# Kernel optimization log

Hardware: AMD Instinct MI355X
Metric: run time of the kernel (lower is better)

## Reference

```python
import jax, jax.numpy as jnp
import numpy as np

NUM_NODES = 94
SEQ_LEN = 784
OUT_CLASSES = 10
ALPHA = 0.5
GAMMA = 0.1
OMEGA = 2.0 * np.pi / 28.0
H = 1.0
INV_SQRT_N = 1.0 / np.sqrt(NUM_NODES)


def _xavier(key, shape):
    fan_in, fan_out = shape[1], shape[0]
    limit = np.sqrt(6.0 / (fan_in + fan_out))
    return jax.random.uniform(key, shape, jnp.float32, -limit, limit)


def setup_inputs() -> dict:
    key = jax.random.key(0)
    k_in, k_ih, k_hh, k_ro = jax.random.split(key, 4)
    batch = 1024
    return {
        "input_sequence": jax.random.normal(k_in, (batch, SEQ_LEN), jnp.float32),
        "w_ih": _xavier(k_ih, (NUM_NODES, 1)),   # Linear(1 -> N) weight
        "b_ih": jnp.zeros((NUM_NODES,), jnp.float32),
        "w_hh": _xavier(k_hh, (NUM_NODES, NUM_NODES)),  # Linear(N -> N) weight
        "b_hh": jnp.zeros((NUM_NODES,), jnp.float32),
        "w_ro": _xavier(k_ro, (OUT_CLASSES, NUM_NODES)),  # readout weight
        "b_ro": jnp.zeros((OUT_CLASSES,), jnp.float32),
    }


def reference(input_sequence, w_ih, b_ih, w_hh, b_hh, w_ro, b_ro):
    batch = input_sequence.shape[0]
    # precompute external drive for all steps: [T, B, N]
    # W_ih(s_t) with input_dim=1 is an outer product: s_t * w_ih[:,0] + b_ih
    s = input_sequence.T  # [T, B]
    w_ih_vec = w_ih[:, 0]  # [N]

    def step(carry, s_t):
        x, y = carry
        I_ext = s_t[:, None] * w_ih_vec[None, :] + b_ih  # [B, N]
        I_rec = y @ w_hh.T + b_hh                        # [B, N]
        A = (I_ext + I_rec) * INV_SQRT_N
        accel = ALPHA * jnp.tanh(A) - 2.0 * GAMMA * y - (OMEGA ** 2) * x
        x_new = x + H * y
        y_new = y + H * accel
        return (x_new, y_new), None

    x0 = jnp.zeros((batch, NUM_NODES), jnp.float32)
    y0 = jnp.zeros((batch, NUM_NODES), jnp.float32)
    (x_final, _), _ = jax.lax.scan(step, (x0, y0), s)
    return x_final @ w_ro.T + b_ro  # [B, 10]
```

## Files before the change

### kernel.cpp

```cpp
#include <hip/hip_runtime.h>
#include <math.h>

#define NUM_NODES 94
#define SEQ_LEN 784
#define OUT_CLASSES 10
#define EPB 16
#define NW 4
#define SP 788
#define YP 104

#define TWO_GAMMA 0.2f
#define OM2 0.0503551324598949f
#define INV_SQRT_N 0.103142124625879
#define LOG2E 1.4426950408889634
#define WSCALE ((float)(2.0 * INV_SQRT_N * LOG2E))

typedef _Float16 half8 __attribute__((ext_vector_type(8)));
typedef _Float16 half4 __attribute__((ext_vector_type(4)));
typedef _Float16 half2v __attribute__((ext_vector_type(2)));
typedef float    floatx4 __attribute__((ext_vector_type(4)));
typedef float    f2 __attribute__((ext_vector_type(2)));

__global__
__attribute__((amdgpu_flat_work_group_size(NW*64, NW*64)))
void horn_kernel(
    const float* __restrict__ input,
    const float* __restrict__ w_ih,
    const float* __restrict__ b_ih,
    const float* __restrict__ w_hh,
    const float* __restrict__ b_hh,
    const float* __restrict__ w_ro,
    const float* __restrict__ b_ro,
    float* __restrict__ out)
{
    __shared__ __align__(16) float    sinl[EPB * SP];
    __shared__ __align__(16) _Float16 ybuf[2][EPB * YP];

    const int tid  = threadIdx.x;
    const int w    = tid >> 6;
    const int lane = tid & 63;
    const int e    = lane & 15;
    const int h    = lane >> 4;
    const int bb   = blockIdx.x;

    const int  S      = 4 + (w >> 1);
    const int  sthalf = w & 1;
    const bool shpub  = ((h >> 1) == sthalf);
    const bool duty   = (w == 0 && h == 3);
    const bool tail53 = (w == 3 && h == 3);

    {
        const floatx4* in4 = (const floatx4*)(input + (size_t)bb * EPB * SEQ_LEN);
        for (int idx = tid; idx < EPB * (SEQ_LEN / 4); idx += NW * 64) {
            int ee = idx / (SEQ_LEN / 4);
            int cc = idx - ee * (SEQ_LEN / 4);
            *(floatx4*)&sinl[ee * SP + 4 * cc] = in4[idx];
        }
    }
    for (int i = tid; i < (2 * EPB * YP) / 2; i += NW * 64) ((float*)ybuf)[i] = 0.0f;
    __syncthreads();
    if (tid < EPB) {
        const float s0 = sinl[tid * SP];
        half2v v; v[0] = (_Float16)s0; v[1] = (_Float16)1.0f;
        *(half2v*)&ybuf[0][tid * YP + NUM_NODES] = v;
    }
    __syncthreads();

    #define LOAD_A(ROW, A0, A1, A2) do {                                           \
        const int arow = (ROW);                                                    \
        _Pragma("unroll")                                                          \
        for (int i = 0; i < 8; ++i) {                                              \
            const int k = 8 * h + i;                                               \
            float v0 = 0.0f, v1 = 0.0f, v2 = 0.0f;                                 \
            if (arow < NUM_NODES) {                                                \
                v0 = w_hh[arow * NUM_NODES + k] * WSCALE;                          \
                v1 = w_hh[arow * NUM_NODES + k + 32] * WSCALE;                     \
                const int k2 = k + 64;                                             \
                if      (k2 <  NUM_NODES) v2 = w_hh[arow * NUM_NODES + k2] * WSCALE; \
                else if (k2 == NUM_NODES) v2 = w_ih[arow] * WSCALE;                \
                else                      v2 = (b_ih[arow] + b_hh[arow]) * WSCALE; \
            }                                                                      \
            (A0)[i] = (_Float16)v0; (A1)[i] = (_Float16)v1; (A2)[i] = (_Float16)v2;\
        }                                                                          \
    } while (0)

    half8 AO0, AO1, AO2, AS0, AS1, AS2;
    LOAD_A(16 * w + e, AO0, AO1, AO2);
    LOAD_A(16 * S + e, AS0, AS1, AS2);
    #undef LOAD_A

    f2 xo01 = {0,0}, xo23 = {0,0}, yo01 = {0,0}, yo23 = {0,0};
    f2 xs01 = {0,0}, xs23 = {0,0}, ys01 = {0,0}, ys23 = {0,0};

    const f2 no2 = {-OM2, -OM2};
    const f2 p82 = {1.0f - TWO_GAMMA, 1.0f - TWO_GAMMA};
    const f2 h05 = {0.5f, 0.5f};
    const floatx4 zf4 = {0,0,0,0};

    #define HSTEP(RP, WP, T_) do {                                                 \
        const _Float16* yb = &ybuf[RP][e * YP + 8 * h];                            \
        half8 B0 = *(const half8*)(yb);                                            \
        half8 B1 = *(const half8*)(yb + 32);                                       \
        half8 B2 = *(const half8*)(yb + 64);                                       \
        float sn = 0.0f;                                                           \
        if (duty) {                                                                \
            const int tn = ((T_) + 1 < SEQ_LEN) ? (T_) + 1 : (SEQ_LEN - 1);        \
            sn = sinl[e * SP + tn];                                                \
        }                                                                          \
                         \
        f2 qo0 = no2 * xo01 + h05;  qo0 = p82 * yo01 + qo0;                        \
        f2 qo1 = no2 * xo23 + h05;  qo1 = p82 * yo23 + qo1;                        \
        f2 qs0 = no2 * xs01 + h05;  qs0 = p82 * ys01 + qs0;                        \
        f2 qs1 = no2 * xs23 + h05;  qs1 = p82 * ys23 + qs1;                        \
        xo01 += yo01;  xo23 += yo23;  xs01 += ys01;  xs23 += ys23;                 \
                                    \
        floatx4 dO  = __builtin_amdgcn_mfma_f32_16x16x32_f16(AO0, B0, zf4, 0, 0, 0); \
        floatx4 dOp = __builtin_amdgcn_mfma_f32_16x16x32_f16(AO1, B1, zf4, 0, 0, 0); \
        floatx4 dS  = __builtin_amdgcn_mfma_f32_16x16x32_f16(AS0, B0, zf4, 0, 0, 0); \
        floatx4 dSp = __builtin_amdgcn_mfma_f32_16x16x32_f16(AS1, B1, zf4, 0, 0, 0); \
        dO = __builtin_amdgcn_mfma_f32_16x16x32_f16(AO2, B2, dO, 0, 0, 0);         \
        dS = __builtin_amdgcn_mfma_f32_16x16x32_f16(AS2, B2, dS, 0, 0, 0);         \
        dO += dOp;  dS += dSp;                          \
        f2 r0, r1;                                                                 \
        r0[0] = __builtin_amdgcn_rcpf(__builtin_amdgcn_exp2f(dO[0]) + 1.0f);       \
        r0[1] = __builtin_amdgcn_rcpf(__builtin_amdgcn_exp2f(dO[1]) + 1.0f);       \
        r1[0] = __builtin_amdgcn_rcpf(__builtin_amdgcn_exp2f(dO[2]) + 1.0f);       \
        r1[1] = __builtin_amdgcn_rcpf(__builtin_amdgcn_exp2f(dO[3]) + 1.0f);       \
        yo01 = qo0 - r0;  yo23 = qo1 - r1;                                         \
        half4 yh;                                                                  \
        yh[0] = (_Float16)yo01[0]; yh[1] = (_Float16)yo01[1];                      \
        yh[2] = (_Float16)yo23[0]; yh[3] = (_Float16)yo23[1];                      \
        *(half4*)&ybuf[WP][e * YP + 16 * w + 4 * h] = yh;       \
        f2 s0_, s1_;                                                               \
        s0_[0] = __builtin_amdgcn_rcpf(__builtin_amdgcn_exp2f(dS[0]) + 1.0f);      \
        s0_[1] = __builtin_amdgcn_rcpf(__builtin_amdgcn_exp2f(dS[1]) + 1.0f);      \
        s1_[0] = __builtin_amdgcn_rcpf(__builtin_amdgcn_exp2f(dS[2]) + 1.0f);      \
        s1_[1] = __builtin_amdgcn_rcpf(__builtin_amdgcn_exp2f(dS[3]) + 1.0f);      \
        ys01 = qs0 - s0_;  ys23 = qs1 - s1_;                                       \
        half4 yhs;                                                                 \
        yhs[0] = (_Float16)ys01[0]; yhs[1] = (_Float16)ys01[1];                    \
        yhs[2] = (_Float16)ys23[0]; yhs[3] = (_Float16)ys23[1];                    \
        if (shpub) {                                                               \
            if (tail53) {                                                          \
                half2v yt; yt[0] = yhs[0]; yt[1] = yhs[1];         \
                *(half2v*)&ybuf[WP][e * YP + 92] = yt;                             \
            } else {                                                               \
                *(half4*)&ybuf[WP][e * YP + 16 * S + 4 * h] = yhs;                 \
            }                                                                      \
        }                                                                          \
        if (duty) {                                                                \
            half2v sv; sv[0] = (_Float16)sn; sv[1] = (_Float16)1.0f;               \
            *(half2v*)&ybuf[WP][e * YP + NUM_NODES] = sv;                          \
        }                                                                          \
        __syncthreads();                                                           \
    } while (0)

    for (int t = 0; t < SEQ_LEN; t += 2) {
        HSTEP(0, 1, t);
        HSTEP(1, 0, t + 1);
    }
    #undef HSTEP

    float* xsh = sinl;
    {
        floatx4 xv;
        xv[0] = xo01[0]; xv[1] = xo01[1]; xv[2] = xo23[0]; xv[3] = xo23[1];
        *(floatx4*)&xsh[e * 100 + 16 * w + 4 * h] = xv;
        if (shpub) {
            floatx4 xw;
            xw[0] = xs01[0]; xw[1] = xs01[1]; xw[2] = xs23[0]; xw[3] = xs23[1];
            *(floatx4*)&xsh[e * 100 + 16 * S + 4 * h] = xw;
        }
    }
    __syncthreads();

    if (tid < EPB * OUT_CLASSES) {
        const int ee = tid / OUT_CLASSES;
        const int c  = tid - ee * OUT_CLASSES;
        float acc = b_ro[c];
        #pragma unroll 2
        for (int r = 0; r < NUM_NODES; ++r)
            acc += xsh[ee * 100 + r] * w_ro[c * NUM_NODES + r];
        out[((size_t)bb * EPB + ee) * OUT_CLASSES + c] = acc;
    }
}

extern "C" void kernel_launch(void* const* d_in, const int* in_sizes, int n_in,
                              void* d_out, int out_size, void* d_ws, size_t ws_size,
                              hipStream_t stream) {
    const float* input = (const float*)d_in[0];
    const float* w_ih  = (const float*)d_in[1];
    const float* b_ih  = (const float*)d_in[2];
    const float* w_hh  = (const float*)d_in[3];
    const float* b_hh  = (const float*)d_in[4];
    const float* w_ro  = (const float*)d_in[5];
    const float* b_ro  = (const float*)d_in[6];
    float* out = (float*)d_out;

    const int batch = in_sizes[0] / SEQ_LEN;
    dim3 grid(batch / EPB);
    dim3 block(NW * 64);

    hipLaunchKernelGGL(horn_kernel, grid, block, 0, stream,
                       input, w_ih, b_ih, w_hh, b_hh, w_ro, b_ro, out);
}
```

Before: 344.6 us.

## Ping-pong two 16-element teams per block to overlap MFMA and tanh phases

Doubles the block to 512 threads with two teams of 16 batch elements each, and alternates the phases. One team runs its MFMA recurrence matmul while the other runs its transcendental/state-update phase, separated by barriers. The goal is to hide the serial latency within each step by interleaving independent work. Input staging now covers half the sequence at a time to fit shared memory, with a global-memory fallback at the boundary. Shared-memory padding is added against bank conflicts, and work for the extra rows is split across waves. The grid is halved, which reduces parallelism across CUs, and the block now pays two barriers per timestep.

```diff
diff --git a/kernel.cpp b/kernel.cpp
--- a/kernel.cpp
+++ b/kernel.cpp
@@ -4,10 +4,11 @@
 #define NUM_NODES 94
 #define SEQ_LEN 784
 #define OUT_CLASSES 10
-#define EPB 16
-#define NW 4
-#define SP 788
+#define EPB 32
+#define SP 396
+#define THALF 392
 #define YP 104
+#define TEAMSZ 1664
 
 #define TWO_GAMMA 0.2f
 #define OM2 0.0503551324598949f
@@ -22,7 +23,7 @@
 typedef float    f2 __attribute__((ext_vector_type(2)));
 
 __global__
-__attribute__((amdgpu_flat_work_group_size(NW*64, NW*64)))
+__attribute__((amdgpu_flat_work_group_size(512, 512)))
 void horn_kernel(
     const float* __restrict__ input,
     const float* __restrict__ w_ih,
@@ -34,7 +35,7 @@
     float* __restrict__ out)
 {
     __shared__ __align__(16) float    sinl[EPB * SP];
-    __shared__ __align__(16) _Float16 ybuf[2][EPB * YP];
+    __shared__ __align__(16) _Float16 ybuf[2 * TEAMSZ];
 
     const int tid  = threadIdx.x;
     const int w    = tid >> 6;
@@ -43,28 +44,34 @@
     const int h    = lane >> 4;
     const int bb   = blockIdx.x;
 
-    const int  S      = 4 + (w >> 1);
-    const int  sthalf = w & 1;
-    const bool shpub  = ((h >> 1) == sthalf);
-    const bool duty   = (w == 0 && h == 3);
-    const bool tail53 = (w == 3 && h == 3);
+    const int  team = w >> 2;
+    const int  ww   = w & 3;
+    const int  S    = 4 + (ww >> 1);
+    const int  p    = ww & 1;
+    const bool duty = (ww == 3 && h == 3);
+
+    const int Eloc = 16 * team + e;
+    _Float16* ybT  = ybuf + team * TEAMSZ;
+    const int eoff = 104 * e + 4 * (e >> 3);
 
     {
-        const floatx4* in4 = (const floatx4*)(input + (size_t)bb * EPB * SEQ_LEN);
-        for (int idx = tid; idx < EPB * (SEQ_LEN / 4); idx += NW * 64) {
-            int ee = idx / (SEQ_LEN / 4);
-            int cc = idx - ee * (SEQ_LEN / 4);
-            *(floatx4*)&sinl[ee * SP + 4 * cc] = in4[idx];
-        }
-    }
-    for (int i = tid; i < (2 * EPB * YP) / 2; i += NW * 64) ((float*)ybuf)[i] = 0.0f;
+        const float* src = input + (size_t)bb * EPB * SEQ_LEN;
+        for (int idx = tid; idx < EPB * (THALF / 4); idx += 512) {
+            int ee = idx / (THALF / 4);
+            int cc = idx - ee * (THALF / 4);
+            *(floatx4*)&sinl[ee * SP + 4 * cc] =
+                *(const floatx4*)(src + (size_t)ee * SEQ_LEN + 4 * cc);
+        }
+    }
+    for (int i = tid; i < (2 * TEAMSZ) / 2; i += 512) ((float*)ybuf)[i] = 0.0f;
     __syncthreads();
     if (tid < EPB) {
+        const int tm = tid >> 4, ee = tid & 15;
+        const int eo = 104 * ee + 4 * (ee >> 3);
         const float s0 = sinl[tid * SP];
         half2v v; v[0] = (_Float16)s0; v[1] = (_Float16)1.0f;
-        *(half2v*)&ybuf[0][tid * YP + NUM_NODES] = v;
-    }
-    __syncthreads();
+        *(half2v*)&ybuf[tm * TEAMSZ + eo + NUM_NODES] = v;
+    }
 
     #define LOAD_A(ROW, A0, A1, A2) do {                                           \
         const int arow = (ROW);                                                    \
@@ -85,91 +92,108 @@
     } while (0)
 
     half8 AO0, AO1, AO2, AS0, AS1, AS2;
-    LOAD_A(16 * w + e, AO0, AO1, AO2);
-    LOAD_A(16 * S + e, AS0, AS1, AS2);
+    LOAD_A(16 * ww + e, AO0, AO1, AO2);
+    LOAD_A(16 * S + e,  AS0, AS1, AS2);
     #undef LOAD_A
 
-    f2 xo01 = {0,0}, xo23 = {0,0}, yo01 = {0,0}, yo23 = {0,0};
-    f2 xs01 = {0,0}, xs23 = {0,0}, ys01 = {0,0}, ys23 = {0,0};
+    f2 x01 = {0,0}, x23 = {0,0}, y01 = {0,0}, y23 = {0,0};
+    f2 xs  = {0,0}, ys  = {0,0};
 
     const f2 no2 = {-OM2, -OM2};
     const f2 p82 = {1.0f - TWO_GAMMA, 1.0f - TWO_GAMMA};
     const f2 h05 = {0.5f, 0.5f};
     const floatx4 zf4 = {0,0,0,0};
-
-    #define HSTEP(RP, WP, T_) do {                                                 \
-        const _Float16* yb = &ybuf[RP][e * YP + 8 * h];                            \
-        half8 B0 = *(const half8*)(yb);                                            \
-        half8 B1 = *(const half8*)(yb + 32);                                       \
-        half8 B2 = *(const half8*)(yb + 64);                                       \
+    floatx4 dO = zf4, dS = zf4;
+
+    #define P0() do {                                                              \
+        const _Float16* yb = &ybT[eoff + 8 * h];                                   \
+        half4 l0 = *(const half4*)(yb);      half4 u0 = *(const half4*)(yb + 4);   \
+        half4 l1 = *(const half4*)(yb + 32); half4 u1 = *(const half4*)(yb + 36);  \
+        half4 l2 = *(const half4*)(yb + 64); half4 u2 = *(const half4*)(yb + 68);  \
+        half8 B0 = __builtin_shufflevector(l0, u0, 0, 1, 2, 3, 4, 5, 6, 7);        \
+        half8 B1 = __builtin_shufflevector(l1, u1, 0, 1, 2, 3, 4, 5, 6, 7);        \
+        half8 B2 = __builtin_shufflevector(l2, u2, 0, 1, 2, 3, 4, 5, 6, 7);        \
+        floatx4 a_ = __builtin_amdgcn_mfma_f32_16x16x32_f16(AO0, B0, zf4, 0, 0, 0);\
+        floatx4 b_ = __builtin_amdgcn_mfma_f32_16x16x32_f16(AO1, B1, zf4, 0, 0, 0);\
+        a_ = __builtin_amdgcn_mfma_f32_16x16x32_f16(AO2, B2, a_, 0, 0, 0);         \
+        dO = a_ + b_;                                                              \
+        floatx4 c_ = __builtin_amdgcn_mfma_f32_16x16x32_f16(AS0, B0, zf4, 0, 0, 0);\
+        floatx4 d_ = __builtin_amdgcn_mfma_f32_16x16x32_f16(AS1, B1, zf4, 0, 0, 0);\
+        c_ = __builtin_amdgcn_mfma_f32_16x16x32_f16(AS2, B2, c_, 0, 0, 0);         \
+        dS = c_ + d_;                                                              \
+    } while (0)
+
+    #define P1(TL, TT) do {                                                        \
+        f2 q0 = no2 * x01 + h05;  q0 = p82 * y01 + q0;                             \
+        f2 q1 = no2 * x23 + h05;  q1 = p82 * y23 + q1;                             \
+        f2 qs = no2 * xs  + h05;  qs = p82 * ys  + qs;                             \
+        x01 += y01;  x23 += y23;  xs += ys;                                        \
         float sn = 0.0f;                                                           \
         if (duty) {                                                                \
-            const int tn = ((T_) + 1 < SEQ_LEN) ? (T_) + 1 : (SEQ_LEN - 1);        \
-            sn = sinl[e * SP + tn];                                                \
+            const int tloc = (TL) + 1;                                             \
+            if (tloc < THALF) sn = sinl[Eloc * SP + tloc];                         \
+            else {                                                                 \
+                const int tg = ((TT) + 1 < SEQ_LEN) ? (TT) + 1 : (SEQ_LEN - 1);    \
+                sn = input[((size_t)bb * EPB + Eloc) * SEQ_LEN + tg];              \
+            }                                                                      \
         }                                                                          \
-                         \
-        f2 qo0 = no2 * xo01 + h05;  qo0 = p82 * yo01 + qo0;                        \
-        f2 qo1 = no2 * xo23 + h05;  qo1 = p82 * yo23 + qo1;                        \
-        f2 qs0 = no2 * xs01 + h05;  qs0 = p82 * ys01 + qs0;                        \
-        f2 qs1 = no2 * xs23 + h05;  qs1 = p82 * ys23 + qs1;                        \
-        xo01 += yo01;  xo23 += yo23;  xs01 += ys01;  xs23 += ys23;                 \
-                                    \
-        floatx4 dO  = __builtin_amdgcn_mfma_f32_16x16x32_f16(AO0, B0, zf4, 0, 0, 0); \
-        floatx4 dOp = __builtin_amdgcn_mfma_f32_16x16x32_f16(AO1, B1, zf4, 0, 0, 0); \
-        floatx4 dS  = __builtin_amdgcn_mfma_f32_16x16x32_f16(AS0, B0, zf4, 0, 0, 0); \
-        floatx4 dSp = __builtin_amdgcn_mfma_f32_16x16x32_f16(AS1, B1, zf4, 0, 0, 0); \
-        dO = __builtin_amdgcn_mfma_f32_16x16x32_f16(AO2, B2, dO, 0, 0, 0);         \
-        dS = __builtin_amdgcn_mfma_f32_16x16x32_f16(AS2, B2, dS, 0, 0, 0);         \
-        dO += dOp;  dS += dSp;                          \
-        f2 r0, r1;                                                                 \
+        f2 dsv;                                                                    \
+        dsv[0] = p ? dS[2] : dS[0];  dsv[1] = p ? dS[3] : dS[1];                   \
+        f2 r0, r1, rs;                                                             \
         r0[0] = __builtin_amdgcn_rcpf(__builtin_amdgcn_exp2f(dO[0]) + 1.0f);       \
         r0[1] = __builtin_amdgcn_rcpf(__builtin_amdgcn_exp2f(dO[1]) + 1.0f);       \
         r1[0] = __builtin_amdgcn_rcpf(__builtin_amdgcn_exp2f(dO[2]) + 1.0f);       \
         r1[1] = __builtin_amdgcn_rcpf(__builtin_amdgcn_exp2f(dO[3]) + 1.0f);       \
-        yo01 = qo0 - r0;  yo23 = qo1 - r1;                                         \
+        rs[0] = __builtin_amdgcn_rcpf(__builtin_amdgcn_exp2f(dsv[0]) + 1.0f);      \
+        rs[1] = __builtin_amdgcn_rcpf(__builtin_amdgcn_exp2f(dsv[1]) + 1.0f);      \
+        y01 = q0 - r0;  y23 = q1 - r1;  ys = qs - rs;                              \
         half4 yh;                                                                  \
-        yh[0] = (_Float16)yo01[0]; yh[1] = (_Float16)yo01[1];                      \
-        yh[2] = (_Float16)yo23[0]; yh[3] = (_Float16)yo23[1];                      \
-        *(half4*)&ybuf[WP][e * YP + 16 * w + 4 * h] = yh;       \
-        f2 s0_, s1_;                                                               \
-        s0_[0] = __builtin_amdgcn_rcpf(__builtin_amdgcn_exp2f(dS[0]) + 1.0f);      \
-        s0_[1] = __builtin_amdgcn_rcpf(__builtin_amdgcn_exp2f(dS[1]) + 1.0f);      \
-        s1_[0] = __builtin_amdgcn_rcpf(__builtin_amdgcn_exp2f(dS[2]) + 1.0f);      \
-        s1_[1] = __builtin_amdgcn_rcpf(__builtin_amdgcn_exp2f(dS[3]) + 1.0f);      \
-        ys01 = qs0 - s0_;  ys23 = qs1 - s1_;                                       \
-        half4 yhs;                                                                 \
-        yhs[0] = (_Float16)ys01[0]; yhs[1] = (_Float16)ys01[1];                    \
-        yhs[2] = (_Float16)ys23[0]; yhs[3] = (_Float16)ys23[1];                    \
-        if (shpub) {                                                               \
-            if (tail53) {                                                          \
-                half2v yt; yt[0] = yhs[0]; yt[1] = yhs[1];         \
-                *(half2v*)&ybuf[WP][e * YP + 92] = yt;                             \
-            } else {                                                               \
-                *(half4*)&ybuf[WP][e * YP + 16 * S + 4 * h] = yhs;                 \
-            }                                                                      \
-        }                                                                          \
+        yh[0] = (_Float16)y01[0]; yh[1] = (_Float16)y01[1];                        \
+        yh[2] = (_Float16)y23[0]; yh[3] = (_Float16)y23[1];                        \
+        *(half4*)&ybT[eoff + 16 * ww + 4 * h] = yh;                                \
         if (duty) {                                                                \
             half2v sv; sv[0] = (_Float16)sn; sv[1] = (_Float16)1.0f;               \
-            *(half2v*)&ybuf[WP][e * YP + NUM_NODES] = sv;                          \
+            *(half2v*)&ybT[eoff + NUM_NODES] = sv;                                 \
+        } else {                                                                   \
+            half2v s2; s2[0] = (_Float16)ys[0]; s2[1] = (_Float16)ys[1];           \
+            *(half2v*)&ybT[eoff + 16 * S + 4 * h + 2 * p] = s2;                    \
         }                                                                          \
-        __syncthreads();                                                           \
     } while (0)
 
-    for (int t = 0; t < SEQ_LEN; t += 2) {
-        HSTEP(0, 1, t);
-        HSTEP(1, 0, t + 1);
-    }
-    #undef HSTEP
+    __syncthreads();
+    if (team == 1) { P0(); }
+    __syncthreads();
+
+    for (int hf = 0; hf < 2; ++hf) {
+        if (hf) {
+            const float* src = input + (size_t)bb * EPB * SEQ_LEN + THALF;
+            for (int idx = tid; idx < EPB * (THALF / 4); idx += 512) {
+                int ee = idx / (THALF / 4);
+                int cc = idx - ee * (THALF / 4);
+                *(floatx4*)&sinl[ee * SP + 4 * cc] =
+                    *(const floatx4*)(src + (size_t)ee * SEQ_LEN + 4 * cc);
+            }
+            __syncthreads();
+        }
+        for (int tl = 0; tl < THALF; ++tl) {
+            const int t = hf * THALF + tl;
+            if (team == 0) P0(); else P1(tl, t);
+            __syncthreads();
+            if (team == 0) P1(tl, t); else if (t + 1 < SEQ_LEN) P0();
+            __syncthreads();
+        }
+    }
+    #undef P0
+    #undef P1
 
     float* xsh = sinl;
     {
         floatx4 xv;
-        xv[0] = xo01[0]; xv[1] = xo01[1]; xv[2] = xo23[0]; xv[3] = xo23[1];
-        *(floatx4*)&xsh[e * 100 + 16 * w + 4 * h] = xv;
-        if (shpub) {
-            floatx4 xw;
-            xw[0] = xs01[0]; xw[1] = xs01[1]; xw[2] = xs23[0]; xw[3] = xs23[1];
-            *(floatx4*)&xsh[e * 100 + 16 * S + 4 * h] = xw;
+        xv[0] = x01[0]; xv[1] = x01[1]; xv[2] = x23[0]; xv[3] = x23[1];
+        *(floatx4*)&xsh[Eloc * 100 + 16 * ww + 4 * h] = xv;
+        if (!duty) {
+            f2 xw = xs;
+            *(f2*)&xsh[Eloc * 100 + 16 * S + 4 * h + 2 * p] = xw;
         }
     }
     __syncthreads();
@@ -199,7 +223,7 @@
 
     const int batch = in_sizes[0] / SEQ_LEN;
     dim3 grid(batch / EPB);
-    dim3 block(NW * 64);
+    dim3 block(512);
 
     hipLaunchKernelGGL(horn_kernel, grid, block, 0, stream,
                        input, w_ih, b_ih, w_hh, b_hh, w_ro, b_ro, out);
```

Measured after the change: 458.9 us. 33.2% more time.
